# Performance work log

Hardware: AMD Instinct MI355X
Metric: run time of the kernel (lower is better)

The kernel has to match this reference:

```python
import jax, jax.numpy as jnp
import numpy as np

N = 8192
IN_F = 512
OUT_F = 256
LEAKY_ALPHA = 0.2
DENSITY = 0.004  # ~32 neighbors per node
NEG_INF = -9e15


def setup_inputs() -> dict:
    key = jax.random.key(0)
    k1, k2, k3, k4 = jax.random.split(key, 4)
    x = jax.random.normal(k1, (N, IN_F), dtype=jnp.float32)
    # sparse random binary adjacency with self-loops
    adj = (jax.random.uniform(k2, (N, N)) < DENSITY).astype(jnp.float32)
    adj = jnp.maximum(adj, jnp.eye(N, dtype=jnp.float32))
    init_range = np.sqrt(6.0 / (IN_F + OUT_F))
    W = jax.random.uniform(k3, (IN_F, OUT_F), dtype=jnp.float32,
                           minval=-init_range, maxval=init_range)
    a_range = np.sqrt(6.0 / (2 * OUT_F + 1))
    a = jax.random.uniform(k4, (2 * OUT_F, 1), dtype=jnp.float32,
                           minval=-a_range, maxval=a_range)
    return {"x": x, "adj": adj, "W": W, "a": a}


def reference(x, adj, W, a):
    h = x @ W                                   # [N, OUT_F]
    a_left, a_right = a[:OUT_F], a[OUT_F:]      # each [OUT_F, 1]
    att_l = h @ a_left                          # [N, 1]
    att_r = h @ a_right                         # [N, 1]
    e = att_l + att_r.T                         # [N, N] additive scores
    e = jax.nn.leaky_relu(e, negative_slope=LEAKY_ALPHA)
    e = jnp.where(adj == 0, NEG_INF, e)         # mask non-edges
    attention = jax.nn.softmax(e, axis=1)       # [N, N]
    # dropout p=0.0 (eval mode): identity
    h_prime = attention @ h                     # [N, OUT_F]
    return jax.nn.elu(h_prime)                  # concat=True -> elu
```

## Files before the change

kernel.cpp:

```cpp
#include <hip/hip_runtime.h>
#include <hip/hip_bf16.h>
#include <math.h>

#define N_NODES 8192
#define IN_F    512
#define OUT_F   256
#define LALPHA  0.2f
#define CAPR    96

#define TM 64
#define TN 64
#define TK 16
#define GEMM_BLOCKS 512

__global__ __launch_bounds__(256) void fused_gemm_scan(const float* __restrict__ X,
                                                       const float* __restrict__ W,
                                                       const float* __restrict__ adj,
                                                       float* __restrict__ H,
                                                       int* __restrict__ csr,
                                                       int* __restrict__ cnts) {
  __shared__ float As[TK][TM + 4];
  __shared__ float Bs[TK][TN];
  __shared__ int   s_cnt;
  __shared__ int   s_idx[CAPR];

  const int b = blockIdx.x;
  const int t = threadIdx.x;

  if (b < GEMM_BLOCKS) {
    const int tx = t & 15;
    const int ty = t >> 4;
    const int r0 = (b & 127) * TM;
    const int c0 = (b >> 7) * TN;

    const int ar  = t >> 2;
    const int akq = t & 3;
    const float* Xp = X + (size_t)(r0 + ar) * IN_F + akq * 4;
    const float* Wp = W + (size_t)ty * OUT_F + c0 + tx * 4;

    float acc[4][4] = {};

    for (int kc = 0; kc < IN_F; kc += TK) {
      const float4 av = *(const float4*)(Xp + kc);
      const float4 bv = *(const float4*)(Wp + (size_t)kc * OUT_F);
      __syncthreads();
      As[akq * 4 + 0][ar] = av.x;
      As[akq * 4 + 1][ar] = av.y;
      As[akq * 4 + 2][ar] = av.z;
      As[akq * 4 + 3][ar] = av.w;
      *(float4*)&Bs[ty][tx * 4] = bv;
      __syncthreads();
#pragma unroll
      for (int kk = 0; kk < TK; ++kk) {
        const float4 a4 = *(const float4*)&As[kk][ty * 4];
        const float4 b4 = *(const float4*)&Bs[kk][tx * 4];
        const float a_[4] = {a4.x, a4.y, a4.z, a4.w};
        const float b_[4] = {b4.x, b4.y, b4.z, b4.w};
#pragma unroll
        for (int i = 0; i < 4; ++i)
#pragma unroll
          for (int j = 0; j < 4; ++j)
            acc[i][j] += a_[i] * b_[j];
      }
    }
#pragma unroll
    for (int i = 0; i < 4; ++i) {
      const float4 o = make_float4(acc[i][0], acc[i][1], acc[i][2], acc[i][3]);
      *(float4*)&H[(size_t)(r0 + ty * 4 + i) * OUT_F + c0 + tx * 4] = o;
    }
  } else {
    const int row = b - GEMM_BLOCKS;
    if (t == 0) s_cnt = 0;
    __syncthreads();
    const float4* arow = (const float4*)(adj + (size_t)row * N_NODES);
#pragma unroll
    for (int q = 0; q < 8; ++q) {
      const int idx4 = t + q * 256;
      const float4 v = arow[idx4];
      const int j0 = idx4 * 4;
      if (v.x != 0.0f) { int p = atomicAdd(&s_cnt, 1); if (p < CAPR) s_idx[p] = j0;     }
      if (v.y != 0.0f) { int p = atomicAdd(&s_cnt, 1); if (p < CAPR) s_idx[p] = j0 + 1; }
      if (v.z != 0.0f) { int p = atomicAdd(&s_cnt, 1); if (p < CAPR) s_idx[p] = j0 + 2; }
      if (v.w != 0.0f) { int p = atomicAdd(&s_cnt, 1); if (p < CAPR) s_idx[p] = j0 + 3; }
    }
    __syncthreads();
    const int cnt = min(s_cnt, CAPR);
    if (t == 0) cnts[row] = cnt;
    if (t < cnt) csr[(size_t)row * CAPR + t] = s_idx[t];
  }
}

__global__ __launch_bounds__(256) void att_proj(const float* __restrict__ H,
                                                const float* __restrict__ a,
                                                float* __restrict__ attl,
                                                float* __restrict__ attr) {
  const int lane = threadIdx.x & 63;
  const int wid  = threadIdx.x >> 6;
  const int row  = blockIdx.x * 4 + wid;
  const float4 hv  = ((const float4*)(H + (size_t)row * OUT_F))[lane];
  const float4 alv = ((const float4*)a)[lane];
  const float4 arv = ((const float4*)(a + OUT_F))[lane];
  float dl = hv.x * alv.x + hv.y * alv.y + hv.z * alv.z + hv.w * alv.w;
  float dr = hv.x * arv.x + hv.y * arv.y + hv.z * arv.z + hv.w * arv.w;
#pragma unroll
  for (int off = 32; off > 0; off >>= 1) {
    dl += __shfl_down(dl, off);
    dr += __shfl_down(dr, off);
  }
  if (lane == 0) { attl[row] = dl; attr[row] = dr; }
}

__global__ __launch_bounds__(256) void attn_agg(const int* __restrict__ csr,
                                                const int* __restrict__ cnts,
                                                const float* __restrict__ H,
                                                const float* __restrict__ attl,
                                                const float* __restrict__ attr,
                                                float* __restrict__ out) {
  __shared__ float s_w[CAPR];
  __shared__ int   s_j[CAPR];
  __shared__ float s_red[4];
  __shared__ float s_invZ;

  const int row  = blockIdx.x;
  const int t    = threadIdx.x;
  const int lane = t & 63;
  const int wid  = t >> 6;

  const int   cnt = cnts[row];
  const float al  = attl[row];

  float w = 0.0f;
  if (t < cnt) {
    const int j = csr[(size_t)row * CAPR + t];
    float e = al + attr[j];
    e = (e > 0.0f) ? e : LALPHA * e;
    w = expf(e);
    s_j[t] = j;
    s_w[t] = w;
  }
#pragma unroll
  for (int off = 32; off > 0; off >>= 1) w += __shfl_down(w, off);
  if (lane == 0) s_red[wid] = w;
  __syncthreads();
  if (t == 0) s_invZ = 1.0f / ((s_red[0] + s_red[1]) + (s_red[2] + s_red[3]));
  __syncthreads();
  const float invZ = s_invZ;

  float acc = 0.0f;
  int k = 0;
  for (; k + 4 <= cnt; k += 4) {
    const float w0 = s_w[k], w1 = s_w[k + 1], w2 = s_w[k + 2], w3 = s_w[k + 3];
    const size_t j0 = (size_t)s_j[k],     j1 = (size_t)s_j[k + 1];
    const size_t j2 = (size_t)s_j[k + 2], j3 = (size_t)s_j[k + 3];
    acc += w0 * H[j0 * OUT_F + t] + w1 * H[j1 * OUT_F + t]
         + w2 * H[j2 * OUT_F + t] + w3 * H[j3 * OUT_F + t];
  }
  for (; k < cnt; ++k)
    acc += s_w[k] * H[(size_t)s_j[k] * OUT_F + t];

  acc *= invZ;
  out[(size_t)row * OUT_F + t] = (acc > 0.0f) ? acc : expm1f(acc);
}

extern "C" void kernel_launch(void* const* d_in, const int* in_sizes, int n_in,
                              void* d_out, int out_size, void* d_ws, size_t ws_size,
                              hipStream_t stream) {
  const float* x   = (const float*)d_in[0];
  const float* adj = (const float*)d_in[1];
  const float* W   = (const float*)d_in[2];
  const float* a   = (const float*)d_in[3];
  float* out = (float*)d_out;

  float* H    = (float*)d_ws;
  float* attl = H + (size_t)N_NODES * OUT_F;
  float* attr = attl + N_NODES;
  int*   cnts = (int*)(attr + N_NODES);
  int*   csr  = cnts + N_NODES;

  fused_gemm_scan<<<GEMM_BLOCKS + N_NODES, 256, 0, stream>>>(x, W, adj, H, csr, cnts);
  att_proj<<<N_NODES / 4, 256, 0, stream>>>(H, a, attl, attr);
  attn_agg<<<N_NODES, 256, 0, stream>>>(csr, cnts, H, attl, attr, out);
}
```

Baseline: 395.9 us.

## Fuse attention projection into GEMM epilogue and use one wave per row in aggregation

The separate att_proj kernel is removed. Each GEMM tile now computes partial dot products of its H tile with a_left and a_right, reduces them across lanes, and accumulates them into attl/attr with atomics after a memset. The aggregation kernel switches from one 256-thread block per row to one wave per row with float4 gathers of H, which removes block-level syncs. This trades one kernel launch and one re-read of H for a memset and global float atomics.

```diff
diff --git a/kernel.cpp b/kernel.cpp
--- a/kernel.cpp
+++ b/kernel.cpp
@@ -15,8 +15,11 @@
 
 __global__ __launch_bounds__(256) void fused_gemm_scan(const float* __restrict__ X,
                                                        const float* __restrict__ W,
+                                                       const float* __restrict__ a,
                                                        const float* __restrict__ adj,
                                                        float* __restrict__ H,
+                                                       float* __restrict__ attl,
+                                                       float* __restrict__ attr,
                                                        int* __restrict__ csr,
                                                        int* __restrict__ cnts) {
   __shared__ float As[TK][TM + 4];
@@ -68,6 +71,22 @@
       const float4 o = make_float4(acc[i][0], acc[i][1], acc[i][2], acc[i][3]);
       *(float4*)&H[(size_t)(r0 + ty * 4 + i) * OUT_F + c0 + tx * 4] = o;
     }
+    const float4 alv = *(const float4*)(a + c0 + tx * 4);
+    const float4 arv = *(const float4*)(a + OUT_F + c0 + tx * 4);
+#pragma unroll
+    for (int i = 0; i < 4; ++i) {
+      float pl = acc[i][0] * alv.x + acc[i][1] * alv.y + acc[i][2] * alv.z + acc[i][3] * alv.w;
+      float pr = acc[i][0] * arv.x + acc[i][1] * arv.y + acc[i][2] * arv.z + acc[i][3] * arv.w;
+#pragma unroll
+      for (int off = 8; off; off >>= 1) {
+        pl += __shfl_down(pl, off);
+        pr += __shfl_down(pr, off);
+      }
+      if (tx == 0) {
+        atomicAdd(&attl[r0 + ty * 4 + i], pl);
+        atomicAdd(&attr[r0 + ty * 4 + i], pr);
+      }
+    }
   } else {
     const int row = b - GEMM_BLOCKS;
     if (t == 0) s_cnt = 0;
@@ -90,76 +109,60 @@
   }
 }
 
-__global__ __launch_bounds__(256) void att_proj(const float* __restrict__ H,
-                                                const float* __restrict__ a,
-                                                float* __restrict__ attl,
-                                                float* __restrict__ attr) {
-  const int lane = threadIdx.x & 63;
-  const int wid  = threadIdx.x >> 6;
-  const int row  = blockIdx.x * 4 + wid;
-  const float4 hv  = ((const float4*)(H + (size_t)row * OUT_F))[lane];
-  const float4 alv = ((const float4*)a)[lane];
-  const float4 arv = ((const float4*)(a + OUT_F))[lane];
-  float dl = hv.x * alv.x + hv.y * alv.y + hv.z * alv.z + hv.w * alv.w;
-  float dr = hv.x * arv.x + hv.y * arv.y + hv.z * arv.z + hv.w * arv.w;
-#pragma unroll
-  for (int off = 32; off > 0; off >>= 1) {
-    dl += __shfl_down(dl, off);
-    dr += __shfl_down(dr, off);
-  }
-  if (lane == 0) { attl[row] = dl; attr[row] = dr; }
-}
-
 __global__ __launch_bounds__(256) void attn_agg(const int* __restrict__ csr,
                                                 const int* __restrict__ cnts,
                                                 const float* __restrict__ H,
                                                 const float* __restrict__ attl,
                                                 const float* __restrict__ attr,
                                                 float* __restrict__ out) {
-  __shared__ float s_w[CAPR];
-  __shared__ int   s_j[CAPR];
-  __shared__ float s_red[4];
-  __shared__ float s_invZ;
+  __shared__ float s_w[4][CAPR];
+  __shared__ int   s_j[4][CAPR];
 
-  const int row  = blockIdx.x;
   const int t    = threadIdx.x;
+  const int wid  = t >> 6;
   const int lane = t & 63;
-  const int wid  = t >> 6;
+  const int row  = blockIdx.x * 4 + wid;
 
   const int   cnt = cnts[row];
   const float al  = attl[row];
 
-  float w = 0.0f;
-  if (t < cnt) {
-    const int j = csr[(size_t)row * CAPR + t];
+  float wsum = 0.0f;
+  for (int k = lane; k < cnt; k += 64) {
+    const int j = csr[(size_t)row * CAPR + k];
     float e = al + attr[j];
     e = (e > 0.0f) ? e : LALPHA * e;
-    w = expf(e);
-    s_j[t] = j;
-    s_w[t] = w;
+    const float w = expf(e);
+    s_j[wid][k] = j;
+    s_w[wid][k] = w;
+    wsum += w;
   }
 #pragma unroll
-  for (int off = 32; off > 0; off >>= 1) w += __shfl_down(w, off);
-  if (lane == 0) s_red[wid] = w;
-  __syncthreads();
-  if (t == 0) s_invZ = 1.0f / ((s_red[0] + s_red[1]) + (s_red[2] + s_red[3]));
-  __syncthreads();
-  const float invZ = s_invZ;
+  for (int off = 32; off > 0; off >>= 1) wsum += __shfl_down(wsum, off);
+  const float invZ = 1.0f / __shfl(wsum, 0);
 
-  float acc = 0.0f;
+  float4 acc = make_float4(0.f, 0.f, 0.f, 0.f);
   int k = 0;
   for (; k + 4 <= cnt; k += 4) {
-    const float w0 = s_w[k], w1 = s_w[k + 1], w2 = s_w[k + 2], w3 = s_w[k + 3];
-    const size_t j0 = (size_t)s_j[k],     j1 = (size_t)s_j[k + 1];
-    const size_t j2 = (size_t)s_j[k + 2], j3 = (size_t)s_j[k + 3];
-    acc += w0 * H[j0 * OUT_F + t] + w1 * H[j1 * OUT_F + t]
-         + w2 * H[j2 * OUT_F + t] + w3 * H[j3 * OUT_F + t];
+#pragma unroll
+    for (int u = 0; u < 4; ++u) {
+      const float  w  = s_w[wid][k + u];
+      const float4 hv = *(const float4*)(H + (size_t)s_j[wid][k + u] * OUT_F + lane * 4);
+      acc.x += w * hv.x; acc.y += w * hv.y; acc.z += w * hv.z; acc.w += w * hv.w;
+    }
   }
-  for (; k < cnt; ++k)
-    acc += s_w[k] * H[(size_t)s_j[k] * OUT_F + t];
+  for (; k < cnt; ++k) {
+    const float  w  = s_w[wid][k];
+    const float4 hv = *(const float4*)(H + (size_t)s_j[wid][k] * OUT_F + lane * 4);
+    acc.x += w * hv.x; acc.y += w * hv.y; acc.z += w * hv.z; acc.w += w * hv.w;
+  }
 
-  acc *= invZ;
-  out[(size_t)row * OUT_F + t] = (acc > 0.0f) ? acc : expm1f(acc);
+  acc.x *= invZ; acc.y *= invZ; acc.z *= invZ; acc.w *= invZ;
+  float4 o;
+  o.x = (acc.x > 0.0f) ? acc.x : expm1f(acc.x);
+  o.y = (acc.y > 0.0f) ? acc.y : expm1f(acc.y);
+  o.z = (acc.z > 0.0f) ? acc.z : expm1f(acc.z);
+  o.w = (acc.w > 0.0f) ? acc.w : expm1f(acc.w);
+  *(float4*)&out[(size_t)row * OUT_F + lane * 4] = o;
 }
 
 extern "C" void kernel_launch(void* const* d_in, const int* in_sizes, int n_in,
@@ -177,7 +180,8 @@
   int*   cnts = (int*)(attr + N_NODES);
   int*   csr  = cnts + N_NODES;
 
-  fused_gemm_scan<<<GEMM_BLOCKS + N_NODES, 256, 0, stream>>>(x, W, adj, H, csr, cnts);
-  att_proj<<<N_NODES / 4, 256, 0, stream>>>(H, a, attl, attr);
-  attn_agg<<<N_NODES, 256, 0, stream>>>(csr, cnts, H, attl, attr, out);
+  hipMemsetAsync(attl, 0, 2 * N_NODES * sizeof(float), stream);
+
+  fused_gemm_scan<<<GEMM_BLOCKS + N_NODES, 256, 0, stream>>>(x, W, a, adj, H, attl, attr, csr, cnts);
+  attn_agg<<<N_NODES / 4, 256, 0, stream>>>(csr, cnts, H, attl, attr, out);
 }
```

After: 392.1 us. About the same (-1.0%).
